# Kernel optimization log

Hardware: AMD Instinct MI355X
Metric: run time of the kernel (lower is better)

Reference implementation:

```python
import jax, jax.numpy as jnp
import numpy as np

SLOPE = 0.1  # LeakyReLU negative slope

def _inv_sqrt(v):
    # pow(v, -0.5) with inf -> 0 (matches torch isinf masking)
    return jnp.where(v > 0, v ** -0.5, 0.0)

def setup_inputs() -> dict:
    key = jax.random.key(0)
    ks = jax.random.split(key, 5)
    P, D, I, H, R = 2048, 4096, 512, 256, 5
    return {
        "p_feat": jax.random.normal(ks[0], (P, I), dtype=jnp.float32),
        "d_feat": jax.random.normal(ks[1], (D, I), dtype=jnp.float32),
        "p": jnp.arange(P, dtype=jnp.int64),
        "d": jnp.arange(D, dtype=jnp.int64),
        "support": jax.random.uniform(ks[2], (R, P, D), dtype=jnp.float32),
        "p_weight": jax.random.normal(ks[3], (R, I, H), dtype=jnp.float32) * (6.0 / (I + H)) ** 0.5,
        "p_bias": jax.random.normal(ks[4], (H,), dtype=jnp.float32),
    }

def reference(p_feat, d_feat, p, d, support, p_weight, p_bias):
    # dropout p=0.0 -> identity (eval semantics)
    # cumulative weight sum across relations: w_cum[r] = sum_{r'<=r} p_weight[r']
    w_cum = jnp.cumsum(p_weight, axis=0)                 # [R, I, H]
    tmp_p = jnp.einsum('pi,rih->rph', p_feat, w_cum)     # [R, P, H]
    tmp_d = jnp.einsum('di,rih->rdh', d_feat, w_cum)     # [R, D, H]

    # normalize(S) = diag(colsum(S)^-1/2) @ S @ diag(rowsum_axis0(S)^-1/2)
    # (torch code builds NxN diags + matmuls; equivalent to broadcast scaling)
    col_scale = _inv_sqrt(support.sum(axis=1))           # [R, D] (sum over P)
    row_scale = _inv_sqrt(support.sum(axis=2))           # [R, P] (sum over D)
    norm = support * row_scale[:, :, None] * col_scale[:, None, :]  # [R, P, D]
    # note: normalize(S.T) == normalize(S).T, so reuse norm for the drug side

    z_p = jnp.einsum('rpd,rdh->ph', norm[:, p, :], tmp_d)   # gather protein rows
    z_d = jnp.einsum('rpd,rph->dh', norm[:, :, d], tmp_p)   # gather drug rows of S.T
    z_p = z_p + p_bias
    z_d = z_d + p_bias  # d_bias is tied to p_bias

    leaky = lambda x: jnp.where(x >= 0, x, SLOPE * x)
    return (leaky(z_p), leaky(z_d))
```

## Files before the change

### kernel.cpp

```cpp
#include <hip/hip_runtime.h>

typedef __bf16 bf16x8 __attribute__((ext_vector_type(8)));
typedef __bf16 bf16x4 __attribute__((ext_vector_type(4)));
typedef float  f32x4  __attribute__((ext_vector_type(4)));

#define P_  2048
#define D_  4096
#define IC_ 512
#define H_  256
#define R_  5
#define KP_ (R_*D_)
#define KD_ (R_*P_)

__device__ __forceinline__ int swz8(int row){ return (row ^ (row>>3)) & 7; }
__device__ __forceinline__ int swzf(int row){ return ((row>>1) ^ (row>>3)) & 3; }

__device__ __forceinline__ bf16x8 cvt8(float4 a, float4 b){
  bf16x8 o;
  o[0]=(__bf16)a.x; o[1]=(__bf16)a.y; o[2]=(__bf16)a.z; o[3]=(__bf16)a.w;
  o[4]=(__bf16)b.x; o[5]=(__bf16)b.y; o[6]=(__bf16)b.z; o[7]=(__bf16)b.w;
  return o;
}

__device__ __forceinline__ void gl_lds16(const __bf16* g, __bf16* l){
  __builtin_amdgcn_global_load_lds(
    (const __attribute__((address_space(1))) unsigned int*)(g),
    (__attribute__((address_space(3))) unsigned int*)(l), 16, 0, 0);
}

__global__ __launch_bounds__(256) void k_prep2(const float* __restrict__ S,
    const float* __restrict__ pw, __bf16* __restrict__ Sbf, float* __restrict__ rs,
    float* __restrict__ cspart, __bf16* __restrict__ wct){
  __shared__ float wsum[32][4];
  const int t = threadIdx.x;
  if (blockIdx.x >= 320){
    const int h  = t;
    const int i0 = (blockIdx.x - 320) * 8;
    float acc[8];
    #pragma unroll
    for (int j=0;j<8;++j) acc[j]=0.f;
    for (int r=0;r<R_;++r){
      bf16x8 o;
      #pragma unroll
      for (int j=0;j<8;++j){
        acc[j] += pw[((size_t)r*IC_ + i0 + j)*H_ + h];
        o[j] = (__bf16)acc[j];
      }
      *reinterpret_cast<bf16x8*>(wct + ((size_t)r*H_ + h)*IC_ + i0) = o;
    }
    return;
  }
  const int lane = t & 63, w = t >> 6;
  const int slab = blockIdx.x;
  const int r = slab >> 6, z = slab & 63;
  const size_t row0 = (size_t)r*P_ + (size_t)z*32;
  const float4* src = reinterpret_cast<const float4*>(S + row0*D_);
  __bf16* dst = Sbf + row0*D_;
  f32x4 ca[4];
  #pragma unroll
  for (int c=0;c<4;++c){ ca[c][0]=0.f; ca[c][1]=0.f; ca[c][2]=0.f; ca[c][3]=0.f; }
  for (int pp=0; pp<32; ++pp){
    float4 v[4];
    #pragma unroll
    for (int c=0;c<4;++c) v[c] = src[(size_t)pp*(D_/4) + t + 256*c];
    float rsum = 0.f;
    #pragma unroll
    for (int c=0;c<4;++c){
      ca[c][0]+=v[c].x; ca[c][1]+=v[c].y; ca[c][2]+=v[c].z; ca[c][3]+=v[c].w;
      rsum += v[c].x+v[c].y+v[c].z+v[c].w;
      bf16x4 o; o[0]=(__bf16)v[c].x; o[1]=(__bf16)v[c].y; o[2]=(__bf16)v[c].z; o[3]=(__bf16)v[c].w;
      *reinterpret_cast<bf16x4*>(dst + (size_t)pp*D_ + (t + 256*c)*4) = o;
    }
    #pragma unroll
    for (int off = 32; off; off >>= 1) rsum += __shfl_xor(rsum, off);
    if (lane == 0) wsum[pp][w] = rsum;
  }
  __syncthreads();
  if (t < 32){
    float s = wsum[t][0]+wsum[t][1]+wsum[t][2]+wsum[t][3];
    rs[row0 + t] = (s > 0.f) ? rsqrtf(s) : 0.f;
  }
  float* o = cspart + ((size_t)z*R_ + r)*D_;
  #pragma unroll
  for (int c=0;c<4;++c) *reinterpret_cast<f32x4*>(o + (t + 256*c)*4) = ca[c];
}

__global__ void k_csfin(const float* __restrict__ cspart, float* __restrict__ cs){
  const int i = blockIdx.x*256 + threadIdx.x;
  float s = 0.f;
  #pragma unroll
  for (int z = 0; z < 64; ++z) s += cspart[(size_t)z*(R_*D_) + i];
  cs[i] = (s > 0.f) ? rsqrtf(s) : 0.f;
}

__global__ __launch_bounds__(256) void k_tmp(const float* __restrict__ p_feat,
    const float* __restrict__ d_feat, const float* __restrict__ rs,
    const float* __restrict__ cs, const __bf16* __restrict__ wct,
    __bf16* __restrict__ Tpt, __bf16* __restrict__ Tdt){
  __shared__ __bf16 As[64*40];
  const int t = threadIdx.x, lane = t & 63, w = t >> 6;
  const int mt = blockIdx.x, r = blockIdx.y;
  const bool isp = mt < (P_/64);
  const float* feat  = isp ? p_feat : d_feat;
  const float* scale = isp ? rs : cs;
  __bf16* outT = isp ? Tpt : Tdt;
  const int M  = isp ? P_ : D_;
  const int RM = isp ? KD_ : KP_;
  const int m0 = (isp ? mt : mt - P_/64)*64;
  const int srow = t >> 2, skc = (t & 3)*8;
  f32x4 acc[4][4];
  #pragma unroll
  for (int a=0;a<4;++a)
    #pragma unroll
    for (int b=0;b<4;++b){ acc[a][b][0]=0.f; acc[a][b][1]=0.f; acc[a][b][2]=0.f; acc[a][b][3]=0.f; }

  for (int ks = 0; ks < IC_; ks += 32){
    __syncthreads();
    {
      const float* g = feat + (size_t)(m0+srow)*IC_ + ks + skc;
      float4 a = *(const float4*)g, b = *(const float4*)(g+4);
      *reinterpret_cast<bf16x8*>(&As[srow*40 + skc]) = cvt8(a,b);
    }
    __syncthreads();
    bf16x8 af[4], bfv[4];
    #pragma unroll
    for (int tt=0;tt<4;++tt)
      af[tt] = *reinterpret_cast<const bf16x8*>(&As[(16*tt + (lane&15))*40 + (lane>>4)*8]);
    #pragma unroll
    for (int cc=0;cc<4;++cc)
      bfv[cc] = *reinterpret_cast<const bf16x8*>(wct + ((size_t)r*H_ + w*64 + 16*cc + (lane&15))*IC_ + ks + (lane>>4)*8);
    #pragma unroll
    for (int tt=0;tt<4;++tt)
      #pragma unroll
      for (int cc=0;cc<4;++cc)
        acc[tt][cc] = __builtin_amdgcn_mfma_f32_16x16x32_bf16(af[tt], bfv[cc], acc[tt][cc], 0, 0, 0);
  }
  #pragma unroll
  for (int tt=0;tt<4;++tt){
    const int mb = m0 + 16*tt + ((lane>>4)<<2);
    const float s0 = scale[r*M+mb+0], s1 = scale[r*M+mb+1],
                s2 = scale[r*M+mb+2], s3 = scale[r*M+mb+3];
    #pragma unroll
    for (int cc=0;cc<4;++cc){
      const int hc = (w<<6) + 16*cc + (lane&15);
      bf16x4 v;
      v[0]=(__bf16)(acc[tt][cc][0]*s0); v[1]=(__bf16)(acc[tt][cc][1]*s1);
      v[2]=(__bf16)(acc[tt][cc][2]*s2); v[3]=(__bf16)(acc[tt][cc][3]*s3);
      *reinterpret_cast<bf16x4*>(outT + (size_t)hc*RM + r*M + mb) = v;
    }
  }
}

__global__ __launch_bounds__(512, 4) void k_z(const __bf16* __restrict__ Sbf,
    const float* __restrict__ rs, const float* __restrict__ cs,
    const __bf16* __restrict__ Tdt, const __bf16* __restrict__ Tpt,
    float* __restrict__ partP, float* __restrict__ partD){
  __shared__ __bf16 As[128*64];
  __shared__ __bf16 Bs[256*64];
  const int t = threadIdx.x, lane = t & 63, w = t >> 6;
  const int wm = w >> 2, wn = w & 3;
  const int bid = blockIdx.x;
  const bool isp = bid < 256;
  const int tile  = isp ? (bid & 15) : ((bid-256) & 31);
  const int split = isp ? (bid >> 4) : ((bid-256) >> 5);
  const int m0 = tile*128;
  const int kbase = split*1280;
  const __bf16* Bsrc = isp ? Tdt : Tpt;
  const int bstr = isp ? KP_ : KD_;
  const int srow = t >> 3, sslot = t & 7;
  const int krow0 = t >> 4, d8 = (t & 15)*8;
  f32x4 acc[4][4];
  #pragma unroll
  for (int a=0;a<4;++a)
    #pragma unroll
    for (int b=0;b<4;++b){ acc[a][b][0]=0.f; acc[a][b][1]=0.f; acc[a][b][2]=0.f; acc[a][b][3]=0.f; }

  for (int ko = 0; ko < 1280; ko += 64){
    const int kg = kbase + ko;
    __syncthreads();
    if (isp){
      const int r = kg >> 12, dd = kg & (D_-1);
      #pragma unroll
      for (int q=0;q<2;++q){
        const int row = q*64 + srow;
        const float sc = rs[r*P_ + m0 + row];
        bf16x8 v = *reinterpret_cast<const bf16x8*>(Sbf + ((size_t)r*P_ + m0 + row)*D_ + dd + sslot*8);
        bf16x8 o;
        #pragma unroll
        for (int j=0;j<8;++j) o[j] = (__bf16)((float)v[j] * sc);
        *reinterpret_cast<bf16x8*>(&As[row*64 + ((sslot ^ swz8(row))<<3)]) = o;
      }
    } else {
      const int r = kg >> 11, pp = kg & (P_-1);
      const float4 c1 = *(const float4*)(cs + r*D_ + m0 + d8);
      const float4 c2 = *(const float4*)(cs + r*D_ + m0 + d8 + 4);
      float cf[8] = {c1.x,c1.y,c1.z,c1.w,c2.x,c2.y,c2.z,c2.w};
      #pragma unroll
      for (int q=0;q<2;++q){
        const int kr = q*32 + krow0;
        bf16x8 va = *reinterpret_cast<const bf16x8*>(Sbf + ((size_t)r*P_ + pp + kr)*D_ + m0 + d8);
        const int slot = kr >> 3, kb = kr & 7;
        #pragma unroll
        for (int j=0;j<8;++j){
          const int rowd = d8 + j;
          As[rowd*64 + ((slot ^ swz8(rowd))<<3) + kb] = (__bf16)((float)va[j] * cf[j]);
        }
      }
    }
    #pragma unroll
    for (int q=0;q<4;++q){
      const int row = q*64 + srow;
      gl_lds16(Bsrc + (size_t)row*bstr + kg + ((sslot ^ swz8(row))<<3), Bs + q*4096 + w*512);
    }
    __syncthreads();
    const int kq = lane >> 4;
    #pragma unroll
    for (int ksub=0; ksub<2; ++ksub){
      const int s = ksub*4 + kq;
      bf16x8 bv[4];
      #pragma unroll
      for (int cc=0;cc<4;++cc){
        const int row = wn*64 + 16*cc + (lane&15);
        bv[cc] = *reinterpret_cast<const bf16x8*>(&Bs[row*64 + ((s ^ swz8(row))<<3)]);
      }
      #pragma unroll
      for (int tt=0;tt<4;++tt){
        const int row = wm*64 + 16*tt + (lane&15);
        bf16x8 af = *reinterpret_cast<const bf16x8*>(&As[row*64 + ((s ^ swz8(row))<<3)]);
        #pragma unroll
        for (int cc=0;cc<4;++cc)
          acc[tt][cc] = __builtin_amdgcn_mfma_f32_16x16x32_bf16(af, bv[cc], acc[tt][cc], 0, 0, 0);
      }
    }
  }
  float* o = isp ? (partP + (size_t)split*((size_t)P_*H_))
                 : (partD + (size_t)split*((size_t)D_*H_));
  #pragma unroll
  for (int tt=0;tt<4;++tt){
    const int mb = m0 + wm*64 + 16*tt + ((lane>>4)<<2);
    #pragma unroll
    for (int cc=0;cc<4;++cc){
      const int hc = wn*64 + 16*cc + (lane&15);
      #pragma unroll
      for (int j=0;j<4;++j) o[(size_t)(mb+j)*H_ + hc] = acc[tt][cc][j];
    }
  }
}

__global__ void k_reduce(const float* __restrict__ partP, const float* __restrict__ partD,
    const float* __restrict__ bias, float* __restrict__ out){
  const int i = (blockIdx.x*256 + threadIdx.x)*4;
  float4 s; s.x=s.y=s.z=s.w=0.f;
  if (i < P_*H_){
    #pragma unroll
    for (int z = 0; z < 16; ++z){
      float4 v = *(const float4*)(partP + (size_t)z*((size_t)P_*H_) + i);
      s.x+=v.x; s.y+=v.y; s.z+=v.z; s.w+=v.w;
    }
  } else {
    const int j = i - P_*H_;
    #pragma unroll
    for (int z = 0; z < 8; ++z){
      float4 v = *(const float4*)(partD + (size_t)z*((size_t)D_*H_) + j);
      s.x+=v.x; s.y+=v.y; s.z+=v.z; s.w+=v.w;
    }
  }
  const float4 b = *(const float4*)(bias + (i & (H_-1)));
  s.x+=b.x; s.y+=b.y; s.z+=b.z; s.w+=b.w;
  s.x = (s.x>=0.f)? s.x : 0.1f*s.x;
  s.y = (s.y>=0.f)? s.y : 0.1f*s.y;
  s.z = (s.z>=0.f)? s.z : 0.1f*s.z;
  s.w = (s.w>=0.f)? s.w : 0.1f*s.w;
  *(float4*)(out + i) = s;
}

extern "C" void kernel_launch(void* const* d_in, const int* in_sizes, int n_in,
                              void* d_out, int out_size, void* d_ws, size_t ws_size,
                              hipStream_t stream){
  (void)in_sizes; (void)n_in; (void)out_size; (void)ws_size;
  const float* p_feat = (const float*)d_in[0];
  const float* d_feat = (const float*)d_in[1];
  const float* S      = (const float*)d_in[4];
  const float* pw     = (const float*)d_in[5];
  const float* bias   = (const float*)d_in[6];
  float* out = (float*)d_out;

  char* ws = (char*)d_ws;
  __bf16* wct    = (__bf16*)(ws + 0);
  __bf16* Tdt    = (__bf16*)(ws + 1310720);
  __bf16* Tpt    = (__bf16*)(ws + 11796480);
  float*  rs     = (float*) (ws + 17039360);
  float*  cs     = (float*) (ws + 17080320);
  float*  cspart = (float*) (ws + 17162240);
  __bf16* Sbf    = (__bf16*)(ws + 22405120);
  float*  partP  = (float*) (ws + 106291200);
  float*  partD  = (float*) (ws + 139845632);

  k_prep2 <<<384, 256, 0, stream>>>(S, pw, Sbf, rs, cspart, wct);
  k_csfin <<<(R_*D_)/256, 256, 0, stream>>>(cspart, cs);
  k_tmp   <<<dim3((P_+D_)/64, R_), 256, 0, stream>>>(p_feat, d_feat, rs, cs, wct, Tpt, Tdt);
  k_z     <<<512, 512, 0, stream>>>(Sbf, rs, cs, Tdt, Tpt, partP, partD);
  k_reduce<<<((P_+D_)*H_)/1024, 256, 0, stream>>>(partP, partD, bias, out);
}
```

Measured before the change: 218.0 us.

## Shrink k_z tiles to 64x256 with K=32 steps and double the grid

Restructures the main z GEMM kernel. The M tile drops from 128 to 64 and the K step from 64 to 32, with each wave now owning a 64x32 output slice. The grid doubles to 1024 blocks and occupancy is raised via launch bounds. Per-relation row/column scales are hoisted out of the K loop, and the LDS swizzle changes to a 4-slot scheme. The aim is more parallelism and smaller LDS/register footprint per block, at the cost of less reuse of the B tile per load, more barriers per FLOP, and half the threads idle during the A load on the protein side.

Result: slower. 245.5 us (+12.6%).

```diff
diff --git a/kernel.cpp b/kernel.cpp
--- a/kernel.cpp
+++ b/kernel.cpp
@@ -12,7 +12,6 @@
 #define KP_ (R_*D_)
 #define KD_ (R_*P_)
 
-__device__ __forceinline__ int swz8(int row){ return (row ^ (row>>3)) & 7; }
 __device__ __forceinline__ int swzf(int row){ return ((row>>1) ^ (row>>3)) & 3; }
 
 __device__ __forceinline__ bf16x8 cvt8(float4 a, float4 b){
@@ -151,96 +150,97 @@
   }
 }
 
-__global__ __launch_bounds__(512, 4) void k_z(const __bf16* __restrict__ Sbf,
+__global__ __launch_bounds__(512, 8) void k_z(const __bf16* __restrict__ Sbf,
     const float* __restrict__ rs, const float* __restrict__ cs,
     const __bf16* __restrict__ Tdt, const __bf16* __restrict__ Tpt,
     float* __restrict__ partP, float* __restrict__ partD){
-  __shared__ __bf16 As[128*64];
-  __shared__ __bf16 Bs[256*64];
+  __shared__ __bf16 As[64*32];
+  __shared__ __bf16 Bs[256*32];
   const int t = threadIdx.x, lane = t & 63, w = t >> 6;
-  const int wm = w >> 2, wn = w & 3;
   const int bid = blockIdx.x;
-  const bool isp = bid < 256;
-  const int tile  = isp ? (bid & 15) : ((bid-256) & 31);
-  const int split = isp ? (bid >> 4) : ((bid-256) >> 5);
-  const int m0 = tile*128;
+  const bool isp = bid < 512;
+  const int tile  = isp ? (bid & 31) : ((bid-512) & 63);
+  const int split = isp ? (bid >> 5) : ((bid-512) >> 6);
+  const int m0 = tile*64;
   const int kbase = split*1280;
   const __bf16* Bsrc = isp ? Tdt : Tpt;
   const int bstr = isp ? KP_ : KD_;
-  const int srow = t >> 3, sslot = t & 7;
-  const int krow0 = t >> 4, d8 = (t & 15)*8;
-  f32x4 acc[4][4];
+  const int arow  = t >> 2;
+  const int aslot = (t & 3) ^ swzf(arow & 63);
+  const int prow = t >> 4, dc4 = (t & 15)*4;
+  const int slotk = prow >> 3, kb = prow & 7;
+  const int brow = t >> 2;
+  const int bko0 = ((t & 3) ^ swzf(brow)) * 8;
+  const int bko1 = ((t & 3) ^ swzf(128 + brow)) * 8;
+  const int rA = isp ? (kbase >> 12) : (kbase >> 11);
+  const int rB = isp ? ((kbase+1279) >> 12) : ((kbase+1279) >> 11);
+  float scA = 0.f, scB = 0.f;
+  float cAf[4], cBf[4];
+  if (isp){
+    if (t < 256){ scA = rs[rA*P_ + m0 + arow]; scB = rs[rB*P_ + m0 + arow]; }
+  } else {
+    float4 a1 = *(const float4*)(cs + rA*D_ + m0 + dc4);
+    float4 b1 = *(const float4*)(cs + rB*D_ + m0 + dc4);
+    cAf[0]=a1.x; cAf[1]=a1.y; cAf[2]=a1.z; cAf[3]=a1.w;
+    cBf[0]=b1.x; cBf[1]=b1.y; cBf[2]=b1.z; cBf[3]=b1.w;
+  }
+
+  f32x4 acc[4][2];
   #pragma unroll
   for (int a=0;a<4;++a)
     #pragma unroll
-    for (int b=0;b<4;++b){ acc[a][b][0]=0.f; acc[a][b][1]=0.f; acc[a][b][2]=0.f; acc[a][b][3]=0.f; }
-
-  for (int ko = 0; ko < 1280; ko += 64){
+    for (int b=0;b<2;++b){ acc[a][b][0]=0.f; acc[a][b][1]=0.f; acc[a][b][2]=0.f; acc[a][b][3]=0.f; }
+
+  for (int ko = 0; ko < 1280; ko += 32){
     const int kg = kbase + ko;
     __syncthreads();
     if (isp){
-      const int r = kg >> 12, dd = kg & (D_-1);
-      #pragma unroll
-      for (int q=0;q<2;++q){
-        const int row = q*64 + srow;
-        const float sc = rs[r*P_ + m0 + row];
-        bf16x8 v = *reinterpret_cast<const bf16x8*>(Sbf + ((size_t)r*P_ + m0 + row)*D_ + dd + sslot*8);
+      if (t < 256){
+        const int r = kg >> 12, dd = kg & (D_-1);
+        const float sc = (r == rA) ? scA : scB;
+        bf16x8 v = *reinterpret_cast<const bf16x8*>(Sbf + ((size_t)r*P_ + m0 + arow)*D_ + dd + (t&3)*8);
         bf16x8 o;
         #pragma unroll
         for (int j=0;j<8;++j) o[j] = (__bf16)((float)v[j] * sc);
-        *reinterpret_cast<bf16x8*>(&As[row*64 + ((sslot ^ swz8(row))<<3)]) = o;
+        *reinterpret_cast<bf16x8*>(&As[arow*32 + aslot*8]) = o;
       }
     } else {
       const int r = kg >> 11, pp = kg & (P_-1);
-      const float4 c1 = *(const float4*)(cs + r*D_ + m0 + d8);
-      const float4 c2 = *(const float4*)(cs + r*D_ + m0 + d8 + 4);
-      float cf[8] = {c1.x,c1.y,c1.z,c1.w,c2.x,c2.y,c2.z,c2.w};
-      #pragma unroll
-      for (int q=0;q<2;++q){
-        const int kr = q*32 + krow0;
-        bf16x8 va = *reinterpret_cast<const bf16x8*>(Sbf + ((size_t)r*P_ + pp + kr)*D_ + m0 + d8);
-        const int slot = kr >> 3, kb = kr & 7;
-        #pragma unroll
-        for (int j=0;j<8;++j){
-          const int rowd = d8 + j;
-          As[rowd*64 + ((slot ^ swz8(rowd))<<3) + kb] = (__bf16)((float)va[j] * cf[j]);
-        }
+      const bool uA = (r == rA);
+      bf16x4 va = *reinterpret_cast<const bf16x4*>(Sbf + ((size_t)r*P_ + pp + prow)*D_ + m0 + dc4);
+      #pragma unroll
+      for (int j=0;j<4;++j){
+        const int rowd = dc4 + j;
+        As[rowd*32 + ((slotk ^ swzf(rowd))<<3) + kb] = (__bf16)((float)va[j] * (uA ? cAf[j] : cBf[j]));
       }
     }
-    #pragma unroll
-    for (int q=0;q<4;++q){
-      const int row = q*64 + srow;
-      gl_lds16(Bsrc + (size_t)row*bstr + kg + ((sslot ^ swz8(row))<<3), Bs + q*4096 + w*512);
-    }
+    gl_lds16(Bsrc + (size_t)brow*bstr       + kg + bko0, Bs + w*512);
+    gl_lds16(Bsrc + (size_t)(128+brow)*bstr + kg + bko1, Bs + 4096 + w*512);
     __syncthreads();
     const int kq = lane >> 4;
-    #pragma unroll
-    for (int ksub=0; ksub<2; ++ksub){
-      const int s = ksub*4 + kq;
-      bf16x8 bv[4];
-      #pragma unroll
-      for (int cc=0;cc<4;++cc){
-        const int row = wn*64 + 16*cc + (lane&15);
-        bv[cc] = *reinterpret_cast<const bf16x8*>(&Bs[row*64 + ((s ^ swz8(row))<<3)]);
-      }
-      #pragma unroll
-      for (int tt=0;tt<4;++tt){
-        const int row = wm*64 + 16*tt + (lane&15);
-        bf16x8 af = *reinterpret_cast<const bf16x8*>(&As[row*64 + ((s ^ swz8(row))<<3)]);
-        #pragma unroll
-        for (int cc=0;cc<4;++cc)
-          acc[tt][cc] = __builtin_amdgcn_mfma_f32_16x16x32_bf16(af, bv[cc], acc[tt][cc], 0, 0, 0);
-      }
+    bf16x8 bv[2];
+    #pragma unroll
+    for (int cc=0;cc<2;++cc){
+      const int row = w*32 + 16*cc + (lane&15);
+      bv[cc] = *reinterpret_cast<const bf16x8*>(&Bs[row*32 + ((kq ^ swzf(row))<<3)]);
+    }
+    #pragma unroll
+    for (int tt=0;tt<4;++tt){
+      const int row = 16*tt + (lane&15);
+      bf16x8 af = *reinterpret_cast<const bf16x8*>(&As[row*32 + ((kq ^ swzf(row))<<3)]);
+      #pragma unroll
+      for (int cc=0;cc<2;++cc)
+        acc[tt][cc] = __builtin_amdgcn_mfma_f32_16x16x32_bf16(af, bv[cc], acc[tt][cc], 0, 0, 0);
     }
   }
   float* o = isp ? (partP + (size_t)split*((size_t)P_*H_))
                  : (partD + (size_t)split*((size_t)D_*H_));
   #pragma unroll
   for (int tt=0;tt<4;++tt){
-    const int mb = m0 + wm*64 + 16*tt + ((lane>>4)<<2);
-    #pragma unroll
-    for (int cc=0;cc<4;++cc){
-      const int hc = wn*64 + 16*cc + (lane&15);
+    const int mb = m0 + 16*tt + ((lane>>4)<<2);
+    #pragma unroll
+    for (int cc=0;cc<2;++cc){
+      const int hc = w*32 + 16*cc + (lane&15);
       #pragma unroll
       for (int j=0;j<4;++j) o[(size_t)(mb+j)*H_ + hc] = acc[tt][cc][j];
     }
@@ -299,6 +299,6 @@
   k_prep2 <<<384, 256, 0, stream>>>(S, pw, Sbf, rs, cspart, wct);
   k_csfin <<<(R_*D_)/256, 256, 0, stream>>>(cspart, cs);
   k_tmp   <<<dim3((P_+D_)/64, R_), 256, 0, stream>>>(p_feat, d_feat, rs, cs, wct, Tpt, Tdt);
-  k_z     <<<512, 512, 0, stream>>>(Sbf, rs, cs, Tdt, Tpt, partP, partD);
+  k_z     <<<1024, 512, 0, stream>>>(Sbf, rs, cs, Tdt, Tpt, partP, partD);
   k_reduce<<<((P_+D_)*H_)/1024, 256, 0, stream>>>(partP, partD, bias, out);
 }
```

## Double-buffer k_z K-loop and move row/col scaling into accumulator epilogue

Applied to the files above, without the earlier changes.

The z-kernel main loop moves from a single 64-wide K tile with two barriers per step to a double-buffered 32-wide tile, so the next B tile (and the next A tile on the drug side) loads while MFMAs run on the current one. The per-element rs/cs scaling of the support matrix is dropped from the inner loop. Scaling is applied to the accumulator instead: it is rescaled by a ratio when the split crosses a relation boundary, and multiplied once in the epilogue. On the protein side A fragments are read straight from global into registers, skipping LDS. The ratio trick relies on at most one relation boundary per split and adds a division that can lose precision for small scale values.

Result: slower. 320.8 us (+47.2%).

```diff
diff --git a/kernel.cpp b/kernel.cpp
--- a/kernel.cpp
+++ b/kernel.cpp
@@ -12,7 +12,6 @@
 #define KP_ (R_*D_)
 #define KD_ (R_*P_)
 
-__device__ __forceinline__ int swz8(int row){ return (row ^ (row>>3)) & 7; }
 __device__ __forceinline__ int swzf(int row){ return ((row>>1) ^ (row>>3)) & 3; }
 
 __device__ __forceinline__ bf16x8 cvt8(float4 a, float4 b){
@@ -155,8 +154,8 @@
     const float* __restrict__ rs, const float* __restrict__ cs,
     const __bf16* __restrict__ Tdt, const __bf16* __restrict__ Tpt,
     float* __restrict__ partP, float* __restrict__ partD){
-  __shared__ __bf16 As[128*64];
-  __shared__ __bf16 Bs[256*64];
+  __shared__ __bf16 As[2][128*32];
+  __shared__ __bf16 Bs[2][256*32];
   const int t = threadIdx.x, lane = t & 63, w = t >> 6;
   const int wm = w >> 2, wn = w & 3;
   const int bid = blockIdx.x;
@@ -167,82 +166,118 @@
   const int kbase = split*1280;
   const __bf16* Bsrc = isp ? Tdt : Tpt;
   const int bstr = isp ? KP_ : KD_;
-  const int srow = t >> 3, sslot = t & 7;
-  const int krow0 = t >> 4, d8 = (t & 15)*8;
+  const float* sv = isp ? rs : cs;
+  const int svdim = isp ? P_ : D_;
+  const int rsh = isp ? 12 : 11;
+  const int rA = kbase >> rsh;
+  const int rB = (kbase + 1279) >> rsh;
+  const int bidx = (rB > rA) ? ((((rA+1) << rsh) - kbase) >> 5) : 999;
+  const int brow0 = t >> 2, brow1 = 128 + brow0;
+  const int bko0 = ((t & 3) ^ swzf(brow0)) * 8;
+  const int bko1 = ((t & 3) ^ swzf(brow1)) * 8;
+  const int prow = t >> 4, d8 = (t & 15)*8;
+  const int kqw = prow >> 3, koff = prow & 7;
+
   f32x4 acc[4][4];
   #pragma unroll
   for (int a=0;a<4;++a)
     #pragma unroll
     for (int b=0;b<4;++b){ acc[a][b][0]=0.f; acc[a][b][1]=0.f; acc[a][b][2]=0.f; acc[a][b][3]=0.f; }
 
-  for (int ko = 0; ko < 1280; ko += 64){
-    const int kg = kbase + ko;
-    __syncthreads();
+  bf16x8 va;
+  if (!isp){
+    const int pp = kbase & (P_-1);
+    va = *reinterpret_cast<const bf16x8*>(Sbf + ((size_t)rA*P_ + pp + prow)*D_ + m0 + d8);
+  }
+  gl_lds16(Bsrc + (size_t)brow0*bstr + kbase + bko0, &Bs[0][w*512]);
+  gl_lds16(Bsrc + (size_t)brow1*bstr + kbase + bko1, &Bs[0][4096 + w*512]);
+  if (!isp){
+    #pragma unroll
+    for (int j=0;j<8;++j){
+      const int rowd = d8 + j;
+      As[0][rowd*32 + ((kqw ^ swzf(rowd))<<3) + koff] = va[j];
+    }
+  }
+
+  int cur = 0;
+  for (int i = 0; i < 40; ++i){
+    const int kg = kbase + 32*i;
+    asm volatile("s_waitcnt vmcnt(0) lgkmcnt(0)" ::: "memory");
+    __builtin_amdgcn_s_barrier();
+    __builtin_amdgcn_sched_barrier(0);
+    if (i == bidx){
+      #pragma unroll
+      for (int tt=0;tt<4;++tt){
+        const int mb = m0 + wm*64 + 16*tt + ((lane>>4)<<2);
+        const float4 sa = *(const float4*)(sv + (size_t)rA*svdim + mb);
+        const float4 sb = *(const float4*)(sv + (size_t)rB*svdim + mb);
+        const float q0 = (sb.x>0.f)?sa.x/sb.x:0.f, q1 = (sb.y>0.f)?sa.y/sb.y:0.f,
+                    q2 = (sb.z>0.f)?sa.z/sb.z:0.f, q3 = (sb.w>0.f)?sa.w/sb.w:0.f;
+        #pragma unroll
+        for (int cc=0;cc<4;++cc){
+          acc[tt][cc][0]*=q0; acc[tt][cc][1]*=q1; acc[tt][cc][2]*=q2; acc[tt][cc][3]*=q3;
+        }
+      }
+    }
+    const int nxt = cur ^ 1;
+    bf16x8 af[4];
     if (isp){
       const int r = kg >> 12, dd = kg & (D_-1);
       #pragma unroll
-      for (int q=0;q<2;++q){
-        const int row = q*64 + srow;
-        const float sc = rs[r*P_ + m0 + row];
-        bf16x8 v = *reinterpret_cast<const bf16x8*>(Sbf + ((size_t)r*P_ + m0 + row)*D_ + dd + sslot*8);
-        bf16x8 o;
-        #pragma unroll
-        for (int j=0;j<8;++j) o[j] = (__bf16)((float)v[j] * sc);
-        *reinterpret_cast<bf16x8*>(&As[row*64 + ((sslot ^ swz8(row))<<3)]) = o;
-      }
-    } else {
-      const int r = kg >> 11, pp = kg & (P_-1);
-      const float4 c1 = *(const float4*)(cs + r*D_ + m0 + d8);
-      const float4 c2 = *(const float4*)(cs + r*D_ + m0 + d8 + 4);
-      float cf[8] = {c1.x,c1.y,c1.z,c1.w,c2.x,c2.y,c2.z,c2.w};
-      #pragma unroll
-      for (int q=0;q<2;++q){
-        const int kr = q*32 + krow0;
-        bf16x8 va = *reinterpret_cast<const bf16x8*>(Sbf + ((size_t)r*P_ + pp + kr)*D_ + m0 + d8);
-        const int slot = kr >> 3, kb = kr & 7;
-        #pragma unroll
-        for (int j=0;j<8;++j){
-          const int rowd = d8 + j;
-          As[rowd*64 + ((slot ^ swz8(rowd))<<3) + kb] = (__bf16)((float)va[j] * cf[j]);
-        }
-      }
-    }
-    #pragma unroll
-    for (int q=0;q<4;++q){
-      const int row = q*64 + srow;
-      gl_lds16(Bsrc + (size_t)row*bstr + kg + ((sslot ^ swz8(row))<<3), Bs + q*4096 + w*512);
-    }
-    __syncthreads();
+      for (int tt=0;tt<4;++tt)
+        af[tt] = *reinterpret_cast<const bf16x8*>(
+          Sbf + ((size_t)r*P_ + m0 + wm*64 + 16*tt + (lane&15))*D_ + dd + (lane>>4)*8);
+    } else if (i+1 < 40){
+      const int kg2 = kg + 32;
+      const int r2 = kg2 >> 11, pp2 = kg2 & (P_-1);
+      va = *reinterpret_cast<const bf16x8*>(Sbf + ((size_t)r2*P_ + pp2 + prow)*D_ + m0 + d8);
+    }
+    if (i+1 < 40){
+      const int kg2 = kg + 32;
+      gl_lds16(Bsrc + (size_t)brow0*bstr + kg2 + bko0, &Bs[nxt][w*512]);
+      gl_lds16(Bsrc + (size_t)brow1*bstr + kg2 + bko1, &Bs[nxt][4096 + w*512]);
+    }
     const int kq = lane >> 4;
-    #pragma unroll
-    for (int ksub=0; ksub<2; ++ksub){
-      const int s = ksub*4 + kq;
-      bf16x8 bv[4];
-      #pragma unroll
-      for (int cc=0;cc<4;++cc){
-        const int row = wn*64 + 16*cc + (lane&15);
-        bv[cc] = *reinterpret_cast<const bf16x8*>(&Bs[row*64 + ((s ^ swz8(row))<<3)]);
-      }
+    bf16x8 bv[4];
+    #pragma unroll
+    for (int cc=0;cc<4;++cc){
+      const int row = wn*64 + 16*cc + (lane&15);
+      bv[cc] = *reinterpret_cast<const bf16x8*>(&Bs[cur][row*32 + ((kq ^ swzf(row))<<3)]);
+    }
+    if (!isp){
       #pragma unroll
       for (int tt=0;tt<4;++tt){
         const int row = wm*64 + 16*tt + (lane&15);
-        bf16x8 af = *reinterpret_cast<const bf16x8*>(&As[row*64 + ((s ^ swz8(row))<<3)]);
-        #pragma unroll
-        for (int cc=0;cc<4;++cc)
-          acc[tt][cc] = __builtin_amdgcn_mfma_f32_16x16x32_bf16(af, bv[cc], acc[tt][cc], 0, 0, 0);
+        af[tt] = *reinterpret_cast<const bf16x8*>(&As[cur][row*32 + ((kq ^ swzf(row))<<3)]);
       }
     }
-  }
+    #pragma unroll
+    for (int tt=0;tt<4;++tt)
+      #pragma unroll
+      for (int cc=0;cc<4;++cc)
+        acc[tt][cc] = __builtin_amdgcn_mfma_f32_16x16x32_bf16(af[tt], bv[cc], acc[tt][cc], 0, 0, 0);
+    if (!isp && i+1 < 40){
+      #pragma unroll
+      for (int j=0;j<8;++j){
+        const int rowd = d8 + j;
+        As[nxt][rowd*32 + ((kqw ^ swzf(rowd))<<3) + koff] = va[j];
+      }
+    }
+    cur = nxt;
+  }
+
   float* o = isp ? (partP + (size_t)split*((size_t)P_*H_))
                  : (partD + (size_t)split*((size_t)D_*H_));
   #pragma unroll
   for (int tt=0;tt<4;++tt){
     const int mb = m0 + wm*64 + 16*tt + ((lane>>4)<<2);
+    const float4 sb = *(const float4*)(sv + (size_t)rB*svdim + mb);
+    const float s4[4] = {sb.x, sb.y, sb.z, sb.w};
     #pragma unroll
     for (int cc=0;cc<4;++cc){
       const int hc = wn*64 + 16*cc + (lane&15);
       #pragma unroll
-      for (int j=0;j<4;++j) o[(size_t)(mb+j)*H_ + hc] = acc[tt][cc][j];
+      for (int j=0;j<4;++j) o[(size_t)(mb+j)*H_ + hc] = acc[tt][cc][j]*s4[j];
     }
   }
 }
```
